# Performance work log

Hardware: AMD Instinct MI355X
Metric: run time of the kernel (lower is better)

The kernel has to match this reference:

```python
import jax, jax.numpy as jnp
import numpy as np

N_NODES = 100000
N_EDGES = 1250000
IN_DIM = 6
HID = 64


def gcn_conv(x, W, b, src, dst, deg_inv_sqrt):
    # x: [N, F_in] -> [N, F_out]; symmetric-normalized aggregation with self-loops
    h = x @ W  # [N, F_out]
    norm = deg_inv_sqrt[src] * deg_inv_sqrt[dst]  # [E]
    msg = h[src] * norm[:, None]                  # gather + scale, [E, F_out]
    agg = jax.ops.segment_sum(msg, dst, num_segments=x.shape[0])
    # self-loop contribution: norm = deg_inv_sqrt[i]^2 = 1/deg[i]
    out = agg + h * (deg_inv_sqrt ** 2)[:, None] + b
    return out


def setup_inputs() -> dict:
    key = jax.random.key(0)
    ks = jax.random.split(key, 8)
    x = jax.random.normal(ks[0], (N_NODES, IN_DIM), dtype=jnp.float32)
    edge_index = jax.random.randint(ks[1], (2, N_EDGES), 0, N_NODES, dtype=jnp.int64)
    s1 = 1.0 / np.sqrt(IN_DIM)
    s2 = 1.0 / np.sqrt(HID)
    W1 = jax.random.uniform(ks[2], (IN_DIM, HID), jnp.float32, -s1, s1)
    b1 = jnp.zeros((HID,), jnp.float32)
    W2 = jax.random.uniform(ks[3], (HID, HID), jnp.float32, -s2, s2)
    b2 = jnp.zeros((HID,), jnp.float32)
    Wfc = jax.random.uniform(ks[4], (HID, 1), jnp.float32, -s2, s2)
    bfc = jnp.zeros((1,), jnp.float32)
    return {"x": x, "edge_index": edge_index, "W1": W1, "b1": b1,
            "W2": W2, "b2": b2, "Wfc": Wfc, "bfc": bfc}


def reference(x, edge_index, W1, b1, W2, b2, Wfc, bfc):
    src, dst = edge_index[0], edge_index[1]
    n = x.shape[0]
    # degree with self-loops (GCN default): in-degree at destination + 1
    deg = jax.ops.segment_sum(jnp.ones((src.shape[0],), x.dtype), dst, num_segments=n) + 1.0
    deg_inv_sqrt = jax.lax.rsqrt(deg)
    h = gcn_conv(x, W1, b1, src, dst, deg_inv_sqrt)
    h = jax.nn.relu(h)
    h = gcn_conv(h, W2, b2, src, dst, deg_inv_sqrt)
    g = h.mean(axis=0)              # [HID] graph readout
    out = jax.nn.sigmoid(g @ Wfc + bfc)  # [1]
    return out
```

## Files before the change

### kernel.cpp

```cpp
#include <hip/hip_runtime.h>
#include <math.h>

#define N_NODES 100000
#define N_EDGES 1250000
#define IN_DIM 6
#define HID 64

#define BIN_SHIFT 8
#define BIN_NODES 256
#define NBIN 391
#define A_BLOCKS 250
#define EPB (N_EDGES / A_BLOCKS)
#define CAP 4096
#define SOFF (NBIN * CAP)

__device__ inline float lo16(unsigned u) { return __uint_as_float(u << 16); }
__device__ inline float hi16(unsigned u) { return __uint_as_float(u & 0xffff0000u); }
__device__ inline unsigned short f2bf(float f) {
    unsigned u = __float_as_uint(f);
    u += 0x7FFFu + ((u >> 16) & 1u);
    return (unsigned short)(u >> 16);
}
__device__ inline unsigned pack2(float a, float b) {
    return (unsigned)f2bf(a) | ((unsigned)f2bf(b) << 16);
}

__global__ __launch_bounds__(1024) void binFill(const int* __restrict__ src,
                                                const int* __restrict__ dst,
                                                int* __restrict__ cnt,
                                                unsigned* __restrict__ rec) {
    __shared__ int lc[NBIN];
    __shared__ int scv[NBIN];
    __shared__ int lb[NBIN];
    __shared__ int lbase[NBIN];
    __shared__ unsigned ldsRec[EPB];
    __shared__ int ldsPos[EPB];

    int t = threadIdx.x;
    int base = blockIdx.x * EPB;

    int4 dA = *(const int4*)&dst[base + t * 4];
    int4 sA = *(const int4*)&src[base + t * 4];
    const int TB = (EPB - 4096) / 4;
    bool hasB = (t < TB);
    int4 dB = make_int4(0, 0, 0, 0), sB = make_int4(0, 0, 0, 0);
    if (hasB) {
        dB = *(const int4*)&dst[base + 4096 + t * 4];
        sB = *(const int4*)&src[base + 4096 + t * 4];
    }

#define HIST4(v4) do {                                  \
        atomicAdd(&lc[(v4).x >> BIN_SHIFT], 1);         \
        atomicAdd(&lc[(v4).y >> BIN_SHIFT], 1);         \
        atomicAdd(&lc[(v4).z >> BIN_SHIFT], 1);         \
        atomicAdd(&lc[(v4).w >> BIN_SHIFT], 1);         \
    } while (0)

#define SCAT1(key, val) do {                                                  \
        int b_ = (key) >> BIN_SHIFT;                                          \
        int loc_ = lbase[b_] + atomicAdd(&lc[b_], 1);                         \
        loc_ = min(loc_, EPB - 1);                                            \
        ldsRec[loc_] = ((unsigned)((key) & (BIN_NODES - 1)) << 17)            \
                     | (unsigned)(val);                                       \
        ldsPos[loc_] = lb[b_] + (loc_ - lbase[b_]);                           \
    } while (0)

#define SCAT4(k4, v4) do {                  \
        SCAT1((k4).x, (v4).x);              \
        SCAT1((k4).y, (v4).y);              \
        SCAT1((k4).z, (v4).z);              \
        SCAT1((k4).w, (v4).w);              \
    } while (0)

#define WRITEOUT() do {                                                       \
        for (int i = t; i < EPB; i += 1024) {                                 \
            unsigned p_ = (unsigned)ldsPos[i];                                \
            if (p_ < (unsigned)(2 * SOFF)) rec[p_] = ldsRec[i];               \
        }                                                                     \
    } while (0)

    if (t < NBIN) lc[t] = 0;
    __syncthreads();
    HIST4(dA);
    if (hasB) HIST4(dB);
    __syncthreads();
    if (t < NBIN) {
        int c = lc[t];
        scv[t] = c;
        lc[t] = 0;
        int off = (c > 0) ? atomicAdd(&cnt[t], c) : 0;
        lb[t] = t * CAP + off;
    }
    __syncthreads();
    if (t < 64) {
        int carry = 0;
#pragma unroll
        for (int cb = 0; cb < NBIN; cb += 64) {
            int idx = cb + t;
            int c = (idx < NBIN) ? scv[idx] : 0;
            int v = c;
#pragma unroll
            for (int off = 1; off < 64; off <<= 1) {
                int u = __shfl_up(v, off, 64);
                if (t >= off) v += u;
            }
            if (idx < NBIN) lbase[idx] = carry + v - c;
            carry += __shfl(v, 63, 64);
        }
    }
    __syncthreads();
    SCAT4(dA, sA);
    if (hasB) SCAT4(dB, sB);
    __syncthreads();
    WRITEOUT();
    __syncthreads();

    if (t < NBIN) lc[t] = 0;
    __syncthreads();
    HIST4(sA);
    if (hasB) HIST4(sB);
    __syncthreads();
    if (t < NBIN) {
        int c = lc[t];
        scv[t] = c;
        lc[t] = 0;
        int off = (c > 0) ? atomicAdd(&cnt[NBIN + t], c) : 0;
        lb[t] = SOFF + t * CAP + off;
    }
    __syncthreads();
    if (t < 64) {
        int carry = 0;
#pragma unroll
        for (int cb = 0; cb < NBIN; cb += 64) {
            int idx = cb + t;
            int c = (idx < NBIN) ? scv[idx] : 0;
            int v = c;
#pragma unroll
            for (int off = 1; off < 64; off <<= 1) {
                int u = __shfl_up(v, off, 64);
                if (t >= off) v += u;
            }
            if (idx < NBIN) lbase[idx] = carry + v - c;
            carry += __shfl(v, 63, 64);
        }
    }
    __syncthreads();
    SCAT4(sA, dA);
    if (hasB) SCAT4(sB, dB);
    __syncthreads();
    WRITEOUT();

#undef HIST4
#undef SCAT1
#undef SCAT4
#undef WRITEOUT
}

__global__ __launch_bounds__(1024) void disXH(const unsigned* __restrict__ rec,
                                              const int* __restrict__ cnt,
                                              const float* __restrict__ x,
                                              int* __restrict__ deg,
                                              float* __restrict__ dis,
                                              uint4* __restrict__ xpad) {
    __shared__ int histS[4][BIN_NODES];
    int t = threadIdx.x, g = t >> 8;
    if (t < 4 * BIN_NODES) ((int*)histS)[t] = 0;
    __syncthreads();
    int bin = blockIdx.x;
    int beg = bin * CAP, end = beg + cnt[bin];
    for (int j = beg + t; j < end; j += 1024) atomicAdd(&histS[g][rec[j] >> 17], 1);
    __syncthreads();
    if (t < BIN_NODES) {
        int n = (bin << BIN_SHIFT) + t;
        if (n < N_NODES) {
            int h = histS[0][t] + histS[1][t] + histS[2][t] + histS[3][t];
            deg[n] = h;
            float d = rsqrtf((float)h + 1.0f);
            dis[n] = d;
            float2 xa = *(const float2*)&x[n * IN_DIM + 0];
            float2 xb = *(const float2*)&x[n * IN_DIM + 2];
            float2 xc = *(const float2*)&x[n * IN_DIM + 4];
            uint4 u;
            u.x = pack2(xa.x * d, xa.y * d);
            u.y = pack2(xb.x * d, xb.y * d);
            u.z = pack2(xc.x * d, xc.y * d);
            u.w = 0;
            xpad[n] = u;
        }
    }
}

__global__ __launch_bounds__(1024) void aggW(const unsigned* __restrict__ rec,
                                             const int* __restrict__ cnt,
                                             const int* __restrict__ deg,
                                             const float* __restrict__ dis,
                                             const uint4* __restrict__ xpad,
                                             const float* __restrict__ W1,
                                             const float* __restrict__ b1,
                                             float* __restrict__ vsum) {
    __shared__ unsigned srcL[CAP];
    __shared__ float wlS[4][BIN_NODES];
    __shared__ int degL[BIN_NODES];
    __shared__ int startS[BIN_NODES];
    __shared__ int cur[BIN_NODES];
    __shared__ int sc[BIN_NODES];
    __shared__ float sAll[BIN_NODES][8];
    __shared__ float w1s[IN_DIM * HID];
    __shared__ float b1s[HID];
    __shared__ float vpart[HID];
    int t = threadIdx.x, g = t >> 8;
    int bin = blockIdx.x;

    if (t < 4 * BIN_NODES) ((float*)wlS)[t] = 0.f;
    if (t < IN_DIM * HID) w1s[t] = W1[t];
    if (t >= 1024 - HID) { int c = t - (1024 - HID); b1s[c] = b1[c]; vpart[c] = 0.f; }
    __syncthreads();

    {
        int beg = SOFF + bin * CAP, end = beg + cnt[NBIN + bin];
        for (int j = beg + t; j < end; j += 1024) {
            unsigned r = rec[j];
            atomicAdd(&wlS[g][r >> 17], dis[r & 131071u]);
        }
    }
    __syncthreads();

    if (t < BIN_NODES) {
        int n = (bin << BIN_SHIFT) + t;
        int h = (n < N_NODES) ? deg[n] : 0;
        degL[t] = h;
        sc[t] = h;
        float d = (n < N_NODES) ? rsqrtf((float)h + 1.0f) : 0.f;
        float wloc = wlS[0][t] + wlS[1][t] + wlS[2][t] + wlS[3][t];
        sAll[t][6] = d;
        sAll[t][7] = (n < N_NODES) ? d * (wloc + d) : 0.f;
    }
    __syncthreads();
    for (int off = 1; off < BIN_NODES; off <<= 1) {
        int add = 0;
        if (t < BIN_NODES && t >= off) add = sc[t - off];
        __syncthreads();
        if (t < BIN_NODES) sc[t] += add;
        __syncthreads();
    }
    if (t < BIN_NODES) {
        int st = sc[t] - degL[t];
        startS[t] = st;
        cur[t] = st;
    }
    __syncthreads();

    {
        int beg = bin * CAP, end = beg + cnt[bin];
        for (int j = beg + t; j < end; j += 1024) {
            unsigned r = rec[j];
            int pos = atomicAdd(&cur[r >> 17], 1);
            if (pos < CAP) srcL[pos] = r & 131071u;
        }
    }
    __syncthreads();

    {
        int node = t >> 2, sub = t & 3;
        int st = startS[node], cn = degL[node];
        int lim = min(st + cn, CAP);
        float s0 = 0.f, s1 = 0.f, s2 = 0.f, s3 = 0.f, s4 = 0.f, s5 = 0.f;
        for (int k = st + sub; k < lim; k += 4) {
            uint4 px = xpad[srcL[k]];
            s0 += lo16(px.x); s1 += hi16(px.x);
            s2 += lo16(px.y); s3 += hi16(px.y);
            s4 += lo16(px.z); s5 += hi16(px.z);
        }
        s0 += __shfl_xor(s0, 1, 64); s0 += __shfl_xor(s0, 2, 64);
        s1 += __shfl_xor(s1, 1, 64); s1 += __shfl_xor(s1, 2, 64);
        s2 += __shfl_xor(s2, 1, 64); s2 += __shfl_xor(s2, 2, 64);
        s3 += __shfl_xor(s3, 1, 64); s3 += __shfl_xor(s3, 2, 64);
        s4 += __shfl_xor(s4, 1, 64); s4 += __shfl_xor(s4, 2, 64);
        s5 += __shfl_xor(s5, 1, 64); s5 += __shfl_xor(s5, 2, 64);
        if (sub == 0) {
            int n = (bin << BIN_SHIFT) + node;
            if (n < N_NODES) {
                uint4 px = xpad[n];
                s0 += lo16(px.x); s1 += hi16(px.x);
                s2 += lo16(px.y); s3 += hi16(px.y);
                s4 += lo16(px.z); s5 += hi16(px.z);
            }
            sAll[node][0] = s0; sAll[node][1] = s1; sAll[node][2] = s2;
            sAll[node][3] = s3; sAll[node][4] = s4; sAll[node][5] = s5;
        }
    }
    __syncthreads();

    {
        int c = t & 63, grp = t >> 6;
        float v = 0.f;
#pragma unroll
        for (int i = 0; i < 16; ++i) {
            int node = grp * 16 + i;
            float d = sAll[node][6], cw = sAll[node][7];
            float a = sAll[node][0] * w1s[0 * HID + c]
                    + sAll[node][1] * w1s[1 * HID + c]
                    + sAll[node][2] * w1s[2 * HID + c]
                    + sAll[node][3] * w1s[3 * HID + c]
                    + sAll[node][4] * w1s[4 * HID + c]
                    + sAll[node][5] * w1s[5 * HID + c];
            v += cw * fmaxf(d * a + b1s[c], 0.f);
        }
        atomicAdd(&vpart[c], v);
    }
    __syncthreads();
    if (t < HID) atomicAdd(&vsum[t], vpart[t]);
}

__global__ void finalK(const float* __restrict__ vsum, const float* __restrict__ W2,
                       const float* __restrict__ b2, const float* __restrict__ Wfc,
                       const float* __restrict__ bfc, float* __restrict__ out) {
    __shared__ float vL[HID];
    int t = threadIdx.x;
    vL[t] = vsum[t] * (1.0f / N_NODES);
    __syncthreads();
    float g = b2[t];
    for (int k = 0; k < HID; ++k) g += vL[k] * W2[k * HID + t];
    float z = g * Wfc[t];
    for (int off = 32; off > 0; off >>= 1) z += __shfl_down(z, off, 64);
    if (t == 0) out[0] = 1.0f / (1.0f + expf(-(z + bfc[0])));
}

extern "C" void kernel_launch(void* const* d_in, const int* in_sizes, int n_in,
                              void* d_out, int out_size, void* d_ws, size_t ws_size,
                              hipStream_t stream) {
    const float* x   = (const float*)d_in[0];
    const int*   ei  = (const int*)d_in[1];
    const float* W1  = (const float*)d_in[2];
    const float* b1  = (const float*)d_in[3];
    const float* W2  = (const float*)d_in[4];
    const float* b2  = (const float*)d_in[5];
    const float* Wfc = (const float*)d_in[6];
    const float* bfc = (const float*)d_in[7];
    const int* src = ei;
    const int* dst = ei + N_EDGES;

    char* ws = (char*)d_ws;
    size_t off = 0;
    auto alloc = (+[](char* base, size_t* o, size_t bytes) {
        char* p = base + *o;
        *o += (bytes + 255) & ~(size_t)255;
        return p;
    });
    int*      cnt  = (int*)     alloc(ws, &off, (size_t)2 * NBIN * 4);
    float*    vsum = (float*)   alloc(ws, &off, 64 * 4);
    uint4*    xpad = (uint4*)   alloc(ws, &off, (size_t)N_NODES * 16);
    float*    dis  = (float*)   alloc(ws, &off, (size_t)N_NODES * 4);
    int*      deg  = (int*)     alloc(ws, &off, (size_t)N_NODES * 4);
    unsigned* rec  = (unsigned*)alloc(ws, &off, (size_t)2 * SOFF * 4);

    hipMemsetAsync(cnt, 0, ((size_t)2 * NBIN * 4 + 255 & ~(size_t)255) + 64 * 4, stream);

    binFill<<<A_BLOCKS, 1024, 0, stream>>>(src, dst, cnt, rec);
    disXH<<<NBIN, 1024, 0, stream>>>(rec, cnt, x, deg, dis, xpad);
    aggW<<<NBIN, 1024, 0, stream>>>(rec, cnt, deg, dis, xpad, W1, b1, vsum);
    finalK<<<1, 64, 0, stream>>>(vsum, W2, b2, Wfc, bfc, (float*)d_out);
}
```

Baseline: 124.0 us.

## Fuse final readout into aggW, halve binFill block size, use wave scan

Removes the separate finalK launch by having the last aggW block, detected through an atomic completion counter, compute the readout matmul and sigmoid. binFill now runs 500 blocks of 512 threads instead of 250 blocks of 1024, so each block bins fewer edges and more blocks can be resident. The multi-barrier LDS prefix scan in aggW is replaced with a single-wave shuffle scan. These changes save a launch and some barriers, at the cost of a threadfence and a global atomic per aggW block.

```diff
diff --git a/kernel.cpp b/kernel.cpp
--- a/kernel.cpp
+++ b/kernel.cpp
@@ -9,8 +9,9 @@
 #define BIN_SHIFT 8
 #define BIN_NODES 256
 #define NBIN 391
-#define A_BLOCKS 250
+#define A_BLOCKS 500
 #define EPB (N_EDGES / A_BLOCKS)
+#define TB2 ((EPB - 2048) / 4)
 #define CAP 4096
 #define SOFF (NBIN * CAP)
 
@@ -25,10 +26,10 @@
     return (unsigned)f2bf(a) | ((unsigned)f2bf(b) << 16);
 }
 
-__global__ __launch_bounds__(1024) void binFill(const int* __restrict__ src,
-                                                const int* __restrict__ dst,
-                                                int* __restrict__ cnt,
-                                                unsigned* __restrict__ rec) {
+__global__ __launch_bounds__(512) void binFill(const int* __restrict__ src,
+                                               const int* __restrict__ dst,
+                                               int* __restrict__ cnt,
+                                               unsigned* __restrict__ rec) {
     __shared__ int lc[NBIN];
     __shared__ int scv[NBIN];
     __shared__ int lb[NBIN];
@@ -41,12 +42,11 @@
 
     int4 dA = *(const int4*)&dst[base + t * 4];
     int4 sA = *(const int4*)&src[base + t * 4];
-    const int TB = (EPB - 4096) / 4;
-    bool hasB = (t < TB);
+    bool hasB = (t < TB2);
     int4 dB = make_int4(0, 0, 0, 0), sB = make_int4(0, 0, 0, 0);
     if (hasB) {
-        dB = *(const int4*)&dst[base + 4096 + t * 4];
-        sB = *(const int4*)&src[base + 4096 + t * 4];
+        dB = *(const int4*)&dst[base + 2048 + t * 4];
+        sB = *(const int4*)&src[base + 2048 + t * 4];
     }
 
 #define HIST4(v4) do {                                  \
@@ -72,8 +72,25 @@
         SCAT1((k4).w, (v4).w);              \
     } while (0)
 
+#define WAVE_SCAN() do {                                                      \
+        if (t < 64) {                                                         \
+            int carry = 0;                                                    \
+            for (int cb = 0; cb < NBIN; cb += 64) {                           \
+                int idx = cb + t;                                             \
+                int c = (idx < NBIN) ? scv[idx] : 0;                          \
+                int v = c;                                                    \
+                for (int off = 1; off < 64; off <<= 1) {                      \
+                    int u = __shfl_up(v, off, 64);                            \
+                    if (t >= off) v += u;                                     \
+                }                                                             \
+                if (idx < NBIN) lbase[idx] = carry + v - c;                   \
+                carry += __shfl(v, 63, 64);                                   \
+            }                                                                 \
+        }                                                                     \
+    } while (0)
+
 #define WRITEOUT() do {                                                       \
-        for (int i = t; i < EPB; i += 1024) {                                 \
+        for (int i = t; i < EPB; i += 512) {                                  \
             unsigned p_ = (unsigned)ldsPos[i];                                \
             if (p_ < (unsigned)(2 * SOFF)) rec[p_] = ldsRec[i];               \
         }                                                                     \
@@ -92,22 +109,7 @@
         lb[t] = t * CAP + off;
     }
     __syncthreads();
-    if (t < 64) {
-        int carry = 0;
-#pragma unroll
-        for (int cb = 0; cb < NBIN; cb += 64) {
-            int idx = cb + t;
-            int c = (idx < NBIN) ? scv[idx] : 0;
-            int v = c;
-#pragma unroll
-            for (int off = 1; off < 64; off <<= 1) {
-                int u = __shfl_up(v, off, 64);
-                if (t >= off) v += u;
-            }
-            if (idx < NBIN) lbase[idx] = carry + v - c;
-            carry += __shfl(v, 63, 64);
-        }
-    }
+    WAVE_SCAN();
     __syncthreads();
     SCAT4(dA, sA);
     if (hasB) SCAT4(dB, sB);
@@ -128,22 +130,7 @@
         lb[t] = SOFF + t * CAP + off;
     }
     __syncthreads();
-    if (t < 64) {
-        int carry = 0;
-#pragma unroll
-        for (int cb = 0; cb < NBIN; cb += 64) {
-            int idx = cb + t;
-            int c = (idx < NBIN) ? scv[idx] : 0;
-            int v = c;
-#pragma unroll
-            for (int off = 1; off < 64; off <<= 1) {
-                int u = __shfl_up(v, off, 64);
-                if (t >= off) v += u;
-            }
-            if (idx < NBIN) lbase[idx] = carry + v - c;
-            carry += __shfl(v, 63, 64);
-        }
-    }
+    WAVE_SCAN();
     __syncthreads();
     SCAT4(sA, dA);
     if (hasB) SCAT4(sB, dB);
@@ -153,6 +140,7 @@
 #undef HIST4
 #undef SCAT1
 #undef SCAT4
+#undef WAVE_SCAN
 #undef WRITEOUT
 }
 
@@ -197,17 +185,23 @@
                                              const uint4* __restrict__ xpad,
                                              const float* __restrict__ W1,
                                              const float* __restrict__ b1,
-                                             float* __restrict__ vsum) {
+                                             const float* __restrict__ W2,
+                                             const float* __restrict__ b2,
+                                             const float* __restrict__ Wfc,
+                                             const float* __restrict__ bfc,
+                                             float* __restrict__ vsum,
+                                             int* __restrict__ done,
+                                             float* __restrict__ out) {
     __shared__ unsigned srcL[CAP];
     __shared__ float wlS[4][BIN_NODES];
     __shared__ int degL[BIN_NODES];
     __shared__ int startS[BIN_NODES];
     __shared__ int cur[BIN_NODES];
-    __shared__ int sc[BIN_NODES];
     __shared__ float sAll[BIN_NODES][8];
     __shared__ float w1s[IN_DIM * HID];
     __shared__ float b1s[HID];
     __shared__ float vpart[HID];
+    __shared__ int lastFlag;
     int t = threadIdx.x, g = t >> 8;
     int bin = blockIdx.x;
 
@@ -229,24 +223,29 @@
         int n = (bin << BIN_SHIFT) + t;
         int h = (n < N_NODES) ? deg[n] : 0;
         degL[t] = h;
-        sc[t] = h;
         float d = (n < N_NODES) ? rsqrtf((float)h + 1.0f) : 0.f;
         float wloc = wlS[0][t] + wlS[1][t] + wlS[2][t] + wlS[3][t];
         sAll[t][6] = d;
         sAll[t][7] = (n < N_NODES) ? d * (wloc + d) : 0.f;
     }
     __syncthreads();
-    for (int off = 1; off < BIN_NODES; off <<= 1) {
-        int add = 0;
-        if (t < BIN_NODES && t >= off) add = sc[t - off];
-        __syncthreads();
-        if (t < BIN_NODES) sc[t] += add;
-        __syncthreads();
-    }
-    if (t < BIN_NODES) {
-        int st = sc[t] - degL[t];
-        startS[t] = st;
-        cur[t] = st;
+    if (t < 64) {
+        int carry = 0;
+#pragma unroll
+        for (int cb = 0; cb < BIN_NODES; cb += 64) {
+            int idx = cb + t;
+            int c = degL[idx];
+            int v = c;
+#pragma unroll
+            for (int off = 1; off < 64; off <<= 1) {
+                int u = __shfl_up(v, off, 64);
+                if (t >= off) v += u;
+            }
+            int st = carry + v - c;
+            startS[idx] = st;
+            cur[idx] = st;
+            carry += __shfl(v, 63, 64);
+        }
     }
     __syncthreads();
 
@@ -310,20 +309,23 @@
     }
     __syncthreads();
     if (t < HID) atomicAdd(&vsum[t], vpart[t]);
-}
-
-__global__ void finalK(const float* __restrict__ vsum, const float* __restrict__ W2,
-                       const float* __restrict__ b2, const float* __restrict__ Wfc,
-                       const float* __restrict__ bfc, float* __restrict__ out) {
-    __shared__ float vL[HID];
-    int t = threadIdx.x;
-    vL[t] = vsum[t] * (1.0f / N_NODES);
-    __syncthreads();
-    float g = b2[t];
-    for (int k = 0; k < HID; ++k) g += vL[k] * W2[k * HID + t];
-    float z = g * Wfc[t];
-    for (int off = 32; off > 0; off >>= 1) z += __shfl_down(z, off, 64);
-    if (t == 0) out[0] = 1.0f / (1.0f + expf(-(z + bfc[0])));
+    __syncthreads();
+
+    if (t == 0) {
+        __threadfence();
+        lastFlag = (atomicAdd(done, 1) == NBIN - 1);
+    }
+    __syncthreads();
+    if (lastFlag && t < 64) {
+        float vv = atomicAdd(&vsum[t], 0.0f) * (1.0f / N_NODES);
+        float gacc = b2[t];
+#pragma unroll 8
+        for (int k = 0; k < HID; ++k)
+            gacc += __shfl(vv, k, 64) * W2[k * HID + t];
+        float z = gacc * Wfc[t];
+        for (int off = 32; off > 0; off >>= 1) z += __shfl_down(z, off, 64);
+        if (t == 0) out[0] = 1.0f / (1.0f + expf(-(z + bfc[0])));
+    }
 }
 
 extern "C" void kernel_launch(void* const* d_in, const int* in_sizes, int n_in,
@@ -349,15 +351,16 @@
     });
     int*      cnt  = (int*)     alloc(ws, &off, (size_t)2 * NBIN * 4);
     float*    vsum = (float*)   alloc(ws, &off, 64 * 4);
+    int*      done = (int*)     alloc(ws, &off, 4);
+    int*      deg  = (int*)     alloc(ws, &off, (size_t)N_NODES * 4);
+    float*    dis  = (float*)   alloc(ws, &off, (size_t)N_NODES * 4);
     uint4*    xpad = (uint4*)   alloc(ws, &off, (size_t)N_NODES * 16);
-    float*    dis  = (float*)   alloc(ws, &off, (size_t)N_NODES * 4);
-    int*      deg  = (int*)     alloc(ws, &off, (size_t)N_NODES * 4);
     unsigned* rec  = (unsigned*)alloc(ws, &off, (size_t)2 * SOFF * 4);
 
-    hipMemsetAsync(cnt, 0, ((size_t)2 * NBIN * 4 + 255 & ~(size_t)255) + 64 * 4, stream);
-
-    binFill<<<A_BLOCKS, 1024, 0, stream>>>(src, dst, cnt, rec);
+    hipMemsetAsync(cnt, 0, (size_t)((char*)deg - (char*)cnt), stream);
+
+    binFill<<<A_BLOCKS, 512, 0, stream>>>(src, dst, cnt, rec);
     disXH<<<NBIN, 1024, 0, stream>>>(rec, cnt, x, deg, dis, xpad);
-    aggW<<<NBIN, 1024, 0, stream>>>(rec, cnt, deg, dis, xpad, W1, b1, vsum);
-    finalK<<<1, 64, 0, stream>>>(vsum, W2, b2, Wfc, bfc, (float*)d_out);
-}
+    aggW<<<NBIN, 1024, 0, stream>>>(rec, cnt, deg, dis, xpad, W1, b1,
+                                    W2, b2, Wfc, bfc, vsum, done, (float*)d_out);
+}
```

After: 136.7 us. +10.2%, slower.
